# Kernel tuning notes

Hardware: AMD Instinct MI355X
Metric: run time of the kernel (lower is better)

Reference implementation:

```python
import jax, jax.numpy as jnp
import numpy as np
import math

N, S, E, H = 32, 64, 512, 4
HD = E // H
EQ = E // 4
L2_TEMP = 13.544
LN_EPS = 1e-5


def _ln(x, g, b):
    m = jnp.mean(x, -1, keepdims=True)
    v = jnp.var(x, -1, keepdims=True)
    return (x - m) * jax.lax.rsqrt(v + LN_EPS) * g + b


def setup_inputs() -> dict:
    key = jax.random.key(0)
    ks = jax.random.split(key, 16)
    sc = 0.02
    inp = {
        "x": jax.random.normal(ks[0], (N, S, E), jnp.float32),
        # MultiheadAttention params (torch layout: in_proj_weight (3E,E))
        "Wqkv": jax.random.normal(ks[1], (3 * E, E), jnp.float32) * sc,
        "bqkv": jnp.zeros((3 * E,), jnp.float32),
        "Wo": jax.random.normal(ks[2], (E, E), jnp.float32) * sc,
        "bo": jnp.zeros((E,), jnp.float32),
        # fc1 (E, 2E), fc2 (E, E)
        "W1": jax.random.normal(ks[3], (E, 2 * E), jnp.float32) * sc,
        "b1": jnp.zeros((E,), jnp.float32),
        "W2": jax.random.normal(ks[4], (E, E), jnp.float32) * sc,
        "b2": jnp.zeros((E,), jnp.float32),
        # layer norms
        "g1": jnp.ones((E,), jnp.float32), "be1": jnp.zeros((E,), jnp.float32),
        "g2": jnp.ones((E,), jnp.float32), "be2": jnp.zeros((E,), jnp.float32),
        # fc_diff1: Linear(E, E//4), Linear(E//4, 1)
        "d1W1": jax.random.normal(ks[5], (EQ, E), jnp.float32) * sc,
        "d1b1": jnp.zeros((EQ,), jnp.float32),
        "d1W2": jax.random.normal(ks[6], (1, EQ), jnp.float32) * sc,
        "d1b2": jnp.zeros((1,), jnp.float32),
        # fc_diff2
        "d2W1": jax.random.normal(ks[7], (EQ, E), jnp.float32) * sc,
        "d2b1": jnp.zeros((EQ,), jnp.float32),
        "d2W2": jax.random.normal(ks[8], (1, EQ), jnp.float32) * sc,
        "d2b2": jnp.zeros((1,), jnp.float32),
    }
    return inp


def _mha(x, Wqkv, bqkv, Wo, bo):
    n, s, e = x.shape
    qkv = x @ Wqkv.T + bqkv
    q, k, v = jnp.split(qkv, 3, axis=-1)
    sh = lambda t: t.reshape(n, s, H, HD).transpose(0, 2, 1, 3)  # (n,H,s,hd)
    q, k, v = sh(q), sh(k), sh(v)
    scores = jnp.einsum('bhqd,bhkd->bhqk', q, k) / math.sqrt(HD)
    a = jax.nn.softmax(scores, axis=-1)
    o = jnp.einsum('bhqk,bhkd->bhqd', a, v).transpose(0, 2, 1, 3).reshape(n, s, e)
    return o @ Wo.T + bo, a.mean(axis=1)  # averaged attn weights (torch default)


def _pair_mlp(diff_w, W1a, b1a, W2a, b2a):
    # F.relu applied after every 'layer' (Linear, Dropout(eval=id), Linear)
    h = jax.nn.relu(diff_w @ W1a.T + b1a)  # relu(dropout(relu)) == relu composed -> same
    return jax.nn.relu(h @ W2a.T + b2a)[..., 0]  # (N,f,f)


def reference(x, Wqkv, bqkv, Wo, bo, W1, b1, W2, b2, g1, be1, g2, be2,
              d1W1, d1b1, d1W2, d1b2, d2W1, d2b1, d2W2, d2b2):
    # diff[b,f,g,e] = x[b,g,e] - x[b,f,e]
    diff = x[:, None, :, :] - x[:, :, None, :]  # (N,f,f,E)
    x1_attn = jax.nn.softmax(-jnp.sum(diff * diff, -1) / L2_TEMP, axis=-1)  # (N,f,f)
    x1 = jnp.einsum('bfg,bge->bfe', x1_attn, x)
    x2, x2_attn = _mha(x, Wqkv, bqkv, Wo, bo)
    x_res = jnp.concatenate([x1, x2], axis=-1)
    h = x + jax.nn.relu(x_res @ W1.T + b1)  # dropout eval = identity
    h = _ln(h, g1, be1)
    h = h + jax.nn.relu(h @ W2.T + b2)
    out = _ln(h, g2, be2)
    diff1 = _pair_mlp(diff * x1_attn[..., None], d1W1, d1b1, d1W2, d1b2)
    diff2 = _pair_mlp(diff * x2_attn[..., None], d2W1, d2b1, d2W2, d2b2)
    return out, x1_attn[:, None], x2_attn[:, None], diff1, diff2
```

## Files before the change

kernel.cpp:

```cpp
#include <hip/hip_runtime.h>
#include <math.h>

#define SS 64
#define EE 512
#define L2T 13.544f
#define LNEPS 1e-5f

using bf16x8 = __attribute__((ext_vector_type(8))) __bf16;
using u16x8  = __attribute__((ext_vector_type(8))) unsigned short;
using f32x4  = __attribute__((ext_vector_type(4))) float;

typedef const void __attribute__((address_space(1))) cv_global;
typedef void __attribute__((address_space(3))) v_lds;

__device__ inline unsigned short f2bf(float f) {
    union { float f; unsigned u; } v; v.f = f;
    unsigned r = v.u + 0x7fff + ((v.u >> 16) & 1);
    return (unsigned short)(r >> 16);
}
__device__ inline float bf2f(unsigned short h) {
    union { unsigned u; float f; } v; v.u = (unsigned)h << 16;
    return v.f;
}

#define XB_O    0
#define WFULL_O 1048576
#define W1CB_O  1966080
#define W2B_O   2490368
#define QKVB_O  2752512
#define X1O_O   5898240
#define HB_O    7995392
#define PB_O    9043968

__global__ __launch_bounds__(256)
void mega1(const float* __restrict__ x, const float* __restrict__ Wqkv,
           const float* __restrict__ Wo, const float* __restrict__ W1,
           const float* __restrict__ W2, const float* __restrict__ d1,
           const float* __restrict__ d2, const float* __restrict__ b1,
           const float* __restrict__ bo, unsigned short* __restrict__ bb,
           float* __restrict__ b_eff, float* __restrict__ x1_attn) {
    const int bx = blockIdx.x, tid = threadIdx.x;
    __shared__ unsigned short ps[5120];
    __shared__ float l2s[128];

    if (bx < 1408) {
        int i = bx * 256 + tid;
        ushort4* dst4 = (ushort4*)bb;
        const float4* s; int di;
        if (i < 196608)      { s = (const float4*)Wqkv + i;          di = WFULL_O/4 + i; }
        else if (i < 212992) { int j = i-196608; s = (const float4*)d1 + j; di = WFULL_O/4 + 196608 + j; }
        else if (i < 229376) { int j = i-212992; s = (const float4*)d2 + j; di = WFULL_O/4 + 212992 + j; }
        else if (i < 294912) { int j = i-229376; s = (const float4*)W2 + j; di = W2B_O/4 + j; }
        else                 { int j = i-294912; int r = j>>7, cq = j&127;
                               s = (const float4*)W1 + r*256 + cq;   di = W1CB_O/4 + r*256 + cq; }
        float4 v = *s;
        ushort4 o;
        o.x = f2bf(v.x); o.y = f2bf(v.y); o.z = f2bf(v.z); o.w = f2bf(v.w);
        dst4[di] = o;
    } else if (bx < 1472) {
        const int tb = bx - 1408;
        const int m0 = (tb >> 3) * 64, n0 = (tb & 7) * 64;
        unsigned short* Asl = ps;
        unsigned short* Bsl = ps + 64 * 40;
        const int wave = tid >> 6, lane = tid & 63;
        const int wm = (wave >> 1) * 32, wn = (wave & 1) * 32;
        const int fr = lane & 15, kq = (lane >> 4) * 8;
        f32x4 acc[2][2] = {};
        for (int k0 = 0; k0 < 512; k0 += 32) {
            {
                int m = tid >> 2, kk = (tid & 3) * 8;
                const float* src = W1 + (size_t)(m0 + m) * 1024 + 512 + k0 + kk;
                float4 v0 = *(const float4*)src, v1 = *(const float4*)(src + 4);
                u16x8 t = {f2bf(v0.x), f2bf(v0.y), f2bf(v0.z), f2bf(v0.w),
                           f2bf(v1.x), f2bf(v1.y), f2bf(v1.z), f2bf(v1.w)};
                *(u16x8*)(Asl + m * 40 + kk) = t;
            }
            {
                int k = tid >> 3, jq = (tid & 7) * 8;
                const float* src = Wo + (size_t)(k0 + k) * 512 + n0 + jq;
                float4 v0 = *(const float4*)src, v1 = *(const float4*)(src + 4);
                float vv[8] = {v0.x, v0.y, v0.z, v0.w, v1.x, v1.y, v1.z, v1.w};
                #pragma unroll
                for (int e = 0; e < 8; ++e) Bsl[(jq + e) * 40 + k] = f2bf(vv[e]);
            }
            __syncthreads();
            bf16x8 a0 = *(const bf16x8*)(Asl + (wm + fr) * 40 + kq);
            bf16x8 a1 = *(const bf16x8*)(Asl + (wm + 16 + fr) * 40 + kq);
            bf16x8 b0 = *(const bf16x8*)(Bsl + (wn + fr) * 40 + kq);
            bf16x8 b1 = *(const bf16x8*)(Bsl + (wn + 16 + fr) * 40 + kq);
            acc[0][0] = __builtin_amdgcn_mfma_f32_16x16x32_bf16(a0, b0, acc[0][0], 0, 0, 0);
            acc[0][1] = __builtin_amdgcn_mfma_f32_16x16x32_bf16(a0, b1, acc[0][1], 0, 0, 0);
            acc[1][0] = __builtin_amdgcn_mfma_f32_16x16x32_bf16(a1, b0, acc[1][0], 0, 0, 0);
            acc[1][1] = __builtin_amdgcn_mfma_f32_16x16x32_bf16(a1, b1, acc[1][1], 0, 0, 0);
            __syncthreads();
        }
        unsigned short* W1cb = bb + W1CB_O;
        const int crow = (lane >> 4) * 4, ccol = lane & 15;
        #pragma unroll
        for (int r2 = 0; r2 < 2; ++r2)
            #pragma unroll
            for (int c2 = 0; c2 < 2; ++c2)
                #pragma unroll
                for (int i = 0; i < 4; ++i) {
                    int m = m0 + wm + r2 * 16 + crow + i;
                    int j = n0 + wn + c2 * 16 + ccol;
                    W1cb[(size_t)m * 1024 + 512 + j] = f2bf(acc[r2][c2][i]);
                }
    } else if (bx < 1476) {
        int n = (bx - 1472) * 128 + (tid >> 1);
        int kh = (tid & 1) * 256;
        float s = 0.f;
        for (int k = 0; k < 256; ++k)
            s += W1[(size_t)n * 1024 + 512 + kh + k] * bo[kh + k];
        s += __shfl_xor(s, 1);
        if ((tid & 1) == 0) b_eff[n] = b1[n] + s;
    } else {
        const int idx = bx - 1476;
        const int b = idx >> 6, f = idx & 63;
        const int wave = tid >> 6, lane = tid & 63;
        float* d2s = l2s; float* attn_s = l2s + 64;

        const float4* xv = (const float4*)(x + (size_t)b * SS * EE);
        float4 xf0 = xv[f * 128 + lane * 2];
        float4 xf1 = xv[f * 128 + lane * 2 + 1];

        for (int g = wave; g < 64; g += 4) {
            float4 a0 = xv[g * 128 + lane * 2];
            float4 a1 = xv[g * 128 + lane * 2 + 1];
            float dx, s = 0.f;
            dx = a0.x - xf0.x; s += dx * dx;
            dx = a0.y - xf0.y; s += dx * dx;
            dx = a0.z - xf0.z; s += dx * dx;
            dx = a0.w - xf0.w; s += dx * dx;
            dx = a1.x - xf1.x; s += dx * dx;
            dx = a1.y - xf1.y; s += dx * dx;
            dx = a1.z - xf1.z; s += dx * dx;
            dx = a1.w - xf1.w; s += dx * dx;
            #pragma unroll
            for (int m = 32; m; m >>= 1) s += __shfl_xor(s, m);
            if (lane == 0) d2s[g] = s;
        }
        __syncthreads();
        if (tid < 64) {
            float v = -d2s[tid] * (1.0f / L2T);
            float mx = v;
            #pragma unroll
            for (int m = 32; m; m >>= 1) mx = fmaxf(mx, __shfl_xor(mx, m));
            float e = expf(v - mx);
            float sum = e;
            #pragma unroll
            for (int m = 32; m; m >>= 1) sum += __shfl_xor(sum, m);
            float a = e / sum;
            x1_attn[((size_t)b * SS + f) * SS + tid] = a;
            attn_s[tid] = a;
        }
        __syncthreads();
        const float* xbf = x + (size_t)b * SS * EE;
        float acc0 = 0.f, acc1 = 0.f;
        #pragma unroll 8
        for (int g = 0; g < 64; ++g) {
            float ag = attn_s[g];
            acc0 += ag * xbf[g * EE + tid];
            acc1 += ag * xbf[g * EE + tid + 256];
        }
        unsigned short* dst = bb + X1O_O + ((size_t)b * SS + f) * 1024;
        dst[tid] = f2bf(acc0);
        dst[tid + 256] = f2bf(acc1);
        unsigned short* xrow = bb + XB_O + ((size_t)b * SS + f) * EE;
        xrow[tid] = f2bf(xbf[f * EE + tid]);
        xrow[tid + 256] = f2bf(xbf[f * EE + tid + 256]);
    }
}

__global__ __launch_bounds__(256)
void gemm_qkvp(const unsigned short* __restrict__ A,
               const unsigned short* __restrict__ B,
               const float* __restrict__ bias,
               unsigned short* __restrict__ Cq, unsigned short* __restrict__ Cp) {
    __shared__ unsigned short Asl[64 * 64];
    __shared__ unsigned short Bsl[64 * 64];
    const int tid = threadIdx.x, wave = tid >> 6, lane = tid & 63;
    const int m0 = blockIdx.y * 64, n0 = blockIdx.x * 64;
    const int wm = (wave >> 1) * 32, wn = (wave & 1) * 32;
    const int fr = lane & 15, kq4 = lane >> 4;
    f32x4 acc[2][2] = {};

    for (int k0 = 0; k0 < 512; k0 += 64) {
        #pragma unroll
        for (int c0 = 0; c0 < 512; c0 += 256) {
            int cc = c0 + tid, r = cc >> 3, q = cc & 7;
            int col = (q ^ (r & 7)) * 8;
            __builtin_amdgcn_global_load_lds(
                (cv_global*)(A + (size_t)(m0 + r) * 512 + k0 + col),
                (v_lds*)(Asl + c0 * 8 + wave * 512), 16, 0, 0);
        }
        #pragma unroll
        for (int c0 = 0; c0 < 512; c0 += 256) {
            int cc = c0 + tid, r = cc >> 3, q = cc & 7;
            int col = (q ^ (r & 7)) * 8;
            __builtin_amdgcn_global_load_lds(
                (cv_global*)(B + (size_t)(n0 + r) * 512 + k0 + col),
                (v_lds*)(Bsl + c0 * 8 + wave * 512), 16, 0, 0);
        }
        __syncthreads();
        #pragma unroll
        for (int j = 0; j < 2; ++j) {
            int kc = kq4 + j * 4;
            int rb0 = wn + fr, rb1 = wn + 16 + fr;
            bf16x8 b0 = *(const bf16x8*)(Bsl + rb0 * 64 + (kc ^ (rb0 & 7)) * 8);
            bf16x8 b1 = *(const bf16x8*)(Bsl + rb1 * 64 + (kc ^ (rb1 & 7)) * 8);
            #pragma unroll
            for (int r = 0; r < 2; ++r) {
                int ra = wm + r * 16 + fr;
                bf16x8 af = *(const bf16x8*)(Asl + ra * 64 + (kc ^ (ra & 7)) * 8);
                acc[r][0] = __builtin_amdgcn_mfma_f32_16x16x32_bf16(af, b0, acc[r][0], 0, 0, 0);
                acc[r][1] = __builtin_amdgcn_mfma_f32_16x16x32_bf16(af, b1, acc[r][1], 0, 0, 0);
            }
        }
        __syncthreads();
    }

    const int crow = (lane >> 4) * 4, ccol = lane & 15;
    if (blockIdx.x < 24) {
        float bj0 = bias[n0 + wn + ccol], bj1 = bias[n0 + wn + 16 + ccol];
        #pragma unroll
        for (int r = 0; r < 2; ++r)
            #pragma unroll
            for (int c = 0; c < 2; ++c) {
                float bj = c ? bj1 : bj0;
                #pragma unroll
                for (int i = 0; i < 4; ++i) {
                    size_t m = (size_t)(m0 + wm + r * 16 + crow + i);
                    int n = n0 + wn + c * 16 + ccol;
                    Cq[m * 1536 + n] = f2bf(acc[r][c][i] + bj);
                }
            }
    } else {
        int p0 = n0 - 1536;
        #pragma unroll
        for (int r = 0; r < 2; ++r)
            #pragma unroll
            for (int c = 0; c < 2; ++c)
                #pragma unroll
                for (int i = 0; i < 4; ++i) {
                    size_t m = (size_t)(m0 + wm + r * 16 + crow + i);
                    int n = p0 + wn + c * 16 + ccol;
                    Cp[m * 256 + n] = f2bf(acc[r][c][i]);
                }
    }
}

__global__ __launch_bounds__(256)
void mha_attn(const unsigned short* __restrict__ qkv,
              unsigned short* __restrict__ x1o, float* __restrict__ pws) {
    const int hh = blockIdx.x;
    const int h = hh >> 1, half = hh & 1;
    const int b = blockIdx.y;
    const int tid = threadIdx.x, wave = tid >> 6, lane = tid & 63;

    __shared__ unsigned short Qs[32 * 136];
    __shared__ unsigned short Ks[64 * 136];
    __shared__ unsigned short Vt[128 * 72];
    __shared__ float sc[32 * 68];
    __shared__ unsigned short Pbf[32 * 72];

    const unsigned short* base = qkv + (size_t)b * 64 * 1536;
    {
        int row = tid >> 3, col = (tid & 7) * 16;
        const unsigned short* src = base + (half * 32 + row) * 1536 + h * 128 + col;
        *(u16x8*)(Qs + row * 136 + col)     = *(const u16x8*)(src);
        *(u16x8*)(Qs + row * 136 + col + 8) = *(const u16x8*)(src + 8);
    }
    {
        int row = tid >> 2, col = (tid & 3) * 32;
        const unsigned short* src = base + row * 1536 + 512 + h * 128 + col;
        #pragma unroll
        for (int j = 0; j < 4; ++j)
            *(u16x8*)(Ks + row * 136 + col + j * 8) = *(const u16x8*)(src + j * 8);
    }
    {
        int g = tid >> 2, col = (tid & 3) * 32;
        const unsigned short* src = base + g * 1536 + 1024 + h * 128 + col;
        #pragma unroll
        for (int j = 0; j < 4; ++j) {
            u16x8 v = *(const u16x8*)(src + j * 8);
            #pragma unroll
            for (int e = 0; e < 8; ++e)
                Vt[(col + j * 8 + e) * 72 + g] = v[e];
        }
    }
    __syncthreads();

    const int fr = lane & 15, kq = (lane >> 4) * 8;
    const int crow = (lane >> 4) * 4, ccol = lane & 15;
    const int wm = (wave >> 1) * 16;
    {
        const int wn = (wave & 1) * 32;
        f32x4 s0 = {0.f, 0.f, 0.f, 0.f}, s1 = s0;
        #pragma unroll
        for (int k0 = 0; k0 < 128; k0 += 32) {
            bf16x8 a  = *(const bf16x8*)(Qs + (wm + fr) * 136 + k0 + kq);
            bf16x8 b0 = *(const bf16x8*)(Ks + (wn + fr) * 136 + k0 + kq);
            bf16x8 b1 = *(const bf16x8*)(Ks + (wn + 16 + fr) * 136 + k0 + kq);
            s0 = __builtin_amdgcn_mfma_f32_16x16x32_bf16(a, b0, s0, 0, 0, 0);
            s1 = __builtin_amdgcn_mfma_f32_16x16x32_bf16(a, b1, s1, 0, 0, 0);
        }
        const float scale = 0.08838834764831845f;
        #pragma unroll
        for (int r = 0; r < 4; ++r) {
            sc[(wm + crow + r) * 68 + wn + ccol]      = s0[r] * scale;
            sc[(wm + crow + r) * 68 + wn + 16 + ccol] = s1[r] * scale;
        }
    }
    __syncthreads();

    #pragma unroll
    for (int i = 0; i < 8; ++i) {
        int f = wave * 8 + i;
        float v = sc[f * 68 + lane];
        float mx = v;
        #pragma unroll
        for (int m = 32; m; m >>= 1) mx = fmaxf(mx, __shfl_xor(mx, m));
        float e = expf(v - mx);
        float sum = e;
        #pragma unroll
        for (int m = 32; m; m >>= 1) sum += __shfl_xor(sum, m);
        float a = e / sum;
        Pbf[f * 72 + lane] = f2bf(a);
        pws[(((size_t)b * 4 + h) * 64 + half * 32 + f) * 64 + lane] = a;
    }
    __syncthreads();

    {
        const int wn2 = (wave & 1) * 64;
        f32x4 o[4];
        #pragma unroll
        for (int t = 0; t < 4; ++t) o[t] = f32x4{0.f, 0.f, 0.f, 0.f};
        #pragma unroll
        for (int k0 = 0; k0 < 64; k0 += 32) {
            bf16x8 a = *(const bf16x8*)(Pbf + (wm + fr) * 72 + k0 + kq);
            #pragma unroll
            for (int t = 0; t < 4; ++t) {
                bf16x8 bv = *(const bf16x8*)(Vt + (wn2 + t * 16 + fr) * 72 + k0 + kq);
                o[t] = __builtin_amdgcn_mfma_f32_16x16x32_bf16(a, bv, o[t], 0, 0, 0);
            }
        }
        #pragma unroll
        for (int t = 0; t < 4; ++t)
            #pragma unroll
            for (int r = 0; r < 4; ++r) {
                size_t m = (size_t)b * 64 + half * 32 + wm + crow + r;
                int col = h * 128 + wn2 + t * 16 + ccol;
                x1o[m * 1024 + 512 + col] = f2bf(o[t][r]);
            }
    }
}

__global__ __launch_bounds__(256)
void w1pair(const unsigned short* __restrict__ x1o,
            const unsigned short* __restrict__ W1cb,
            const float* __restrict__ beff, float* __restrict__ u,
            const unsigned short* __restrict__ Pb,
            const float* __restrict__ a1, const float* __restrict__ pws,
            const float* __restrict__ d1b1, const float* __restrict__ d1w2,
            const float* __restrict__ d1b2, const float* __restrict__ d2b1,
            const float* __restrict__ d2w2, const float* __restrict__ d2b2,
            float* __restrict__ x2_attn, float* __restrict__ out1,
            float* __restrict__ out2) {
    __shared__ unsigned short Asl[32 * 64];
    __shared__ unsigned short Bsl[64 * 64];
    const int bx = blockIdx.x, tid = threadIdx.x;
    const int wave = tid >> 6, lane = tid & 63;

    if (bx < 512) {
        const int m0 = (bx >> 3) * 32, n0 = (bx & 7) * 64;
        const int wm = (wave >> 1) * 16, wn = (wave & 1) * 32;
        const int fr = lane & 15, kq4 = lane >> 4;
        f32x4 acc[2] = {};
        for (int k0 = 0; k0 < 1024; k0 += 64) {
            {
                int r = tid >> 3, q = tid & 7;
                int col = (q ^ (r & 7)) * 8;
                __builtin_amdgcn_global_load_lds(
                    (cv_global*)(x1o + (size_t)(m0 + r) * 1024 + k0 + col),
                    (v_lds*)(Asl + wave * 512), 16, 0, 0);
            }
            #pragma unroll
            for (int c0 = 0; c0 < 512; c0 += 256) {
                int cc = c0 + tid, r = cc >> 3, q = cc & 7;
                int col = (q ^ (r & 7)) * 8;
                __builtin_amdgcn_global_load_lds(
                    (cv_global*)(W1cb + (size_t)(n0 + r) * 1024 + k0 + col),
                    (v_lds*)(Bsl + c0 * 8 + wave * 512), 16, 0, 0);
            }
            __syncthreads();
            #pragma unroll
            for (int j = 0; j < 2; ++j) {
                int kc = kq4 + j * 4;
                int rb0 = wn + fr, rb1 = wn + 16 + fr, ra = wm + fr;
                bf16x8 b0 = *(const bf16x8*)(Bsl + rb0 * 64 + (kc ^ (rb0 & 7)) * 8);
                bf16x8 b1 = *(const bf16x8*)(Bsl + rb1 * 64 + (kc ^ (rb1 & 7)) * 8);
                bf16x8 af = *(const bf16x8*)(Asl + ra * 64 + (kc ^ (ra & 7)) * 8);
                acc[0] = __builtin_amdgcn_mfma_f32_16x16x32_bf16(af, b0, acc[0], 0, 0, 0);
                acc[1] = __builtin_amdgcn_mfma_f32_16x16x32_bf16(af, b1, acc[1], 0, 0, 0);
            }
            __syncthreads();
        }
        const int crow = (lane >> 4) * 4, ccol = lane & 15;
        #pragma unroll
        for (int c = 0; c < 2; ++c) {
            int n = n0 + wn + c * 16 + ccol;
            float bj = beff[n];
            #pragma unroll
            for (int i = 0; i < 4; ++i) {
                size_t m = (size_t)(m0 + wm + crow + i);
                u[m * 512 + n] = fmaxf(acc[c][i] + bj, 0.f);
            }
        }
    } else {
        const int idx = bx - 512;
        const int f = idx & 63, b = idx >> 6;
        const size_t row = (size_t)b * SS + f;
        const int c0 = lane * 2, c1 = lane * 2 + 1;

        const float p1f0 = bf2f(Pb[row * 256 + c0]),       p1f1 = bf2f(Pb[row * 256 + c1]);
        const float p2f0 = bf2f(Pb[row * 256 + 128 + c0]), p2f1 = bf2f(Pb[row * 256 + 128 + c1]);
        const float w10 = d1w2[c0], w11 = d1w2[c1];
        const float w20 = d2w2[c0], w21 = d2w2[c1];
        const float b10 = d1b1[c0], b11 = d1b1[c1];
        const float b20 = d2b1[c0], b21 = d2b1[c1];
        const float bb1 = d1b2[0], bb2 = d2b2[0];

        const float* a1r = a1 + row * SS;
        const float* ph0 = pws + (((size_t)b * 4 + 0) * 64 + f) * 64;
        const float* ph1 = pws + (((size_t)b * 4 + 1) * 64 + f) * 64;
        const float* ph2 = pws + (((size_t)b * 4 + 2) * 64 + f) * 64;
        const float* ph3 = pws + (((size_t)b * 4 + 3) * 64 + f) * 64;
        const size_t bbase = (size_t)b * SS * 256;

        for (int g = wave; g < 64; g += 4) {
            float aa1 = a1r[g];
            float aa2 = 0.25f * (ph0[g] + ph1[g] + ph2[g] + ph3[g]);
            float q10 = bf2f(Pb[bbase + g * 256 + c0]);
            float q11 = bf2f(Pb[bbase + g * 256 + c1]);
            float q20 = bf2f(Pb[bbase + g * 256 + 128 + c0]);
            float q21 = bf2f(Pb[bbase + g * 256 + 128 + c1]);
            float h10 = fmaxf(aa1 * (q10 - p1f0) + b10, 0.f);
            float h11 = fmaxf(aa1 * (q11 - p1f1) + b11, 0.f);
            float h20 = fmaxf(aa2 * (q20 - p2f0) + b20, 0.f);
            float h21 = fmaxf(aa2 * (q21 - p2f1) + b21, 0.f);
            float s1 = w10 * h10 + w11 * h11;
            float s2 = w20 * h20 + w21 * h21;
            #pragma unroll
            for (int m = 32; m; m >>= 1) {
                s1 += __shfl_xor(s1, m);
                s2 += __shfl_xor(s2, m);
            }
            if (lane == 0) {
                x2_attn[row * SS + g] = aa2;
                out1[row * SS + g] = fmaxf(s1 + bb1, 0.f);
                out2[row * SS + g] = fmaxf(s2 + bb2, 0.f);
            }
        }
    }
}

__global__ __launch_bounds__(256)
void gemm_w2(const unsigned short* __restrict__ A,
             const unsigned short* __restrict__ B,
             const float* __restrict__ bias, float* __restrict__ C) {
    __shared__ unsigned short Asl[32 * 64];
    __shared__ unsigned short Bsl[64 * 64];
    const int tid = threadIdx.x, wave = tid >> 6, lane = tid & 63;
    const int m0 = blockIdx.y * 32, n0 = blockIdx.x * 64;
    const int wm = (wave >> 1) * 16, wn = (wave & 1) * 32;
    const int fr = lane & 15, kq4 = lane >> 4;
    f32x4 acc[2] = {};
    for (int k0 = 0; k0 < 512; k0 += 64) {
        {
            int r = tid >> 3, q = tid & 7;
            int col = (q ^ (r & 7)) * 8;
            __builtin_amdgcn_global_load_lds(
                (cv_global*)(A + (size_t)(m0 + r) * 512 + k0 + col),
                (v_lds*)(Asl + wave * 512), 16, 0, 0);
        }
        #pragma unroll
        for (int c0 = 0; c0 < 512; c0 += 256) {
            int cc = c0 + tid, r = cc >> 3, q = cc & 7;
            int col = (q ^ (r & 7)) * 8;
            __builtin_amdgcn_global_load_lds(
                (cv_global*)(B + (size_t)(n0 + r) * 512 + k0 + col),
                (v_lds*)(Bsl + c0 * 8 + wave * 512), 16, 0, 0);
        }
        __syncthreads();
        #pragma unroll
        for (int j = 0; j < 2; ++j) {
            int kc = kq4 + j * 4;
            int rb0 = wn + fr, rb1 = wn + 16 + fr, ra = wm + fr;
            bf16x8 b0 = *(const bf16x8*)(Bsl + rb0 * 64 + (kc ^ (rb0 & 7)) * 8);
            bf16x8 b1 = *(const bf16x8*)(Bsl + rb1 * 64 + (kc ^ (rb1 & 7)) * 8);
            bf16x8 af = *(const bf16x8*)(Asl + ra * 64 + (kc ^ (ra & 7)) * 8);
            acc[0] = __builtin_amdgcn_mfma_f32_16x16x32_bf16(af, b0, acc[0], 0, 0, 0);
            acc[1] = __builtin_amdgcn_mfma_f32_16x16x32_bf16(af, b1, acc[1], 0, 0, 0);
        }
        __syncthreads();
    }
    const int crow = (lane >> 4) * 4, ccol = lane & 15;
    #pragma unroll
    for (int c = 0; c < 2; ++c) {
        int n = n0 + wn + c * 16 + ccol;
        float bj = bias[n];
        #pragma unroll
        for (int i = 0; i < 4; ++i) {
            size_t m = (size_t)(m0 + wm + crow + i);
            C[m * 512 + n] = fmaxf(acc[c][i] + bj, 0.f);
        }
    }
}

__global__ __launch_bounds__(256)
void add_ln(const float* __restrict__ base, const float* __restrict__ u,
            const float* __restrict__ gam, const float* __restrict__ bet,
            float* __restrict__ out, unsigned short* __restrict__ outb) {
    const int row = blockIdx.x;
    const int tid = threadIdx.x, wave = tid >> 6, lane = tid & 63;
    const float* br = base + (size_t)row * EE;
    const float* ur = u + (size_t)row * EE;
    float t0 = br[tid] + ur[tid];
    float t1 = br[tid + 256] + ur[tid + 256];
    float s = t0 + t1, sq = t0 * t0 + t1 * t1;
    #pragma unroll
    for (int m = 32; m; m >>= 1) {
        s += __shfl_xor(s, m);
        sq += __shfl_xor(sq, m);
    }
    __shared__ float ssum[4], ssq[4];
    if (lane == 0) { ssum[wave] = s; ssq[wave] = sq; }
    __syncthreads();
    s = ssum[0] + ssum[1] + ssum[2] + ssum[3];
    sq = ssq[0] + ssq[1] + ssq[2] + ssq[3];
    float mean = s * (1.0f / EE);
    float var = sq * (1.0f / EE) - mean * mean;
    float inv = rsqrtf(var + LNEPS);
    float v0 = (t0 - mean) * inv * gam[tid] + bet[tid];
    float v1 = (t1 - mean) * inv * gam[tid + 256] + bet[tid + 256];
    float* orow = out + (size_t)row * EE;
    orow[tid] = v0;
    orow[tid + 256] = v1;
    if (outb) {
        unsigned short* obr = outb + (size_t)row * EE;
        obr[tid] = f2bf(v0);
        obr[tid + 256] = f2bf(v1);
    }
}

extern "C" void kernel_launch(void* const* d_in, const int* in_sizes, int n_in,
                              void* d_out, int out_size, void* d_ws,
                              size_t ws_size, hipStream_t stream) {
    const float* x    = (const float*)d_in[0];
    const float* Wqkv = (const float*)d_in[1];
    const float* bqkv = (const float*)d_in[2];
    const float* Wo   = (const float*)d_in[3];
    const float* bo   = (const float*)d_in[4];
    const float* W1   = (const float*)d_in[5];
    const float* b1   = (const float*)d_in[6];
    const float* W2   = (const float*)d_in[7];
    const float* b2   = (const float*)d_in[8];
    const float* g1   = (const float*)d_in[9];
    const float* be1  = (const float*)d_in[10];
    const float* g2   = (const float*)d_in[11];
    const float* be2  = (const float*)d_in[12];
    const float* d1W1 = (const float*)d_in[13];
    const float* d1b1 = (const float*)d_in[14];
    const float* d1W2 = (const float*)d_in[15];
    const float* d1b2 = (const float*)d_in[16];
    const float* d2W1 = (const float*)d_in[17];
    const float* d2b1 = (const float*)d_in[18];
    const float* d2W2 = (const float*)d_in[19];
    const float* d2b2 = (const float*)d_in[20];

    float* out      = (float*)d_out;
    float* out_main = out;
    float* x1_attn  = out + 1048576;
    float* x2_attn  = out + 1048576 + 131072;
    float* diff1    = out + 1048576 + 2 * 131072;
    float* diff2    = out + 1048576 + 3 * 131072;

    float* ws    = (float*)d_ws;
    float* u_buf = ws;
    float* h_buf = ws + 1048576;
    float* pws   = ws + 2097152;
    float* b_eff = ws + 2621440;
    unsigned short* bb = (unsigned short*)(ws + 2621952);

    unsigned short* xb    = bb + XB_O;
    unsigned short* Wfull = bb + WFULL_O;
    unsigned short* W1cb  = bb + W1CB_O;
    unsigned short* W2b   = bb + W2B_O;
    unsigned short* qkvb  = bb + QKVB_O;
    unsigned short* x1o   = bb + X1O_O;
    unsigned short* hb    = bb + HB_O;
    unsigned short* Pb    = bb + PB_O;

    mega1<<<3524, 256, 0, stream>>>(x, Wqkv, Wo, W1, W2, d1W1, d2W1, b1, bo,
                                    bb, b_eff, x1_attn);

    gemm_qkvp<<<dim3(28, 32), 256, 0, stream>>>(xb, Wfull, bqkv, qkvb, Pb);

    mha_attn<<<dim3(8, 32), 256, 0, stream>>>(qkvb, x1o, pws);

    w1pair<<<2560, 256, 0, stream>>>(x1o, W1cb, b_eff, u_buf, Pb, x1_attn, pws,
                                     d1b1, d1W2, d1b2, d2b1, d2W2, d2b2,
                                     x2_attn, diff1, diff2);

    add_ln<<<2048, 256, 0, stream>>>(x, u_buf, g1, be1, h_buf, hb);

    gemm_w2<<<dim3(8, 64), 256, 0, stream>>>(hb, W2b, b2, u_buf);

    add_ln<<<2048, 256, 0, stream>>>(h_buf, u_buf, g2, be2, out_main, nullptr);
}
```

Before: 191.2 us.

## Compute L2 attention via split-bf16 Gram MFMA and move x1 matmul into QKV kernel

The pairwise squared-distance path now runs one block per batch. It builds the 64x64 Gram matrix of x with MFMA, splitting each value into hi and lo bf16 parts (three products) to keep precision, and forms distances as norm_f + norm_g - 2*dot. This replaces 2048 per-row blocks that each reread the batch's rows from global memory. The softmax weights are stored as bf16, and the attention-weighted sum x1 = attn @ x is computed by extra MFMA blocks in the QKV GEMM launch. The cost is some precision loss from the norm expansion and bf16 weights, and a larger shared-memory footprint per block.

```diff
diff --git a/kernel.cpp b/kernel.cpp
--- a/kernel.cpp
+++ b/kernel.cpp
@@ -22,6 +22,8 @@
     union { unsigned u; float f; } v; v.u = (unsigned)h << 16;
     return v.f;
 }
+
+#define MFMA16 __builtin_amdgcn_mfma_f32_16x16x32_bf16
 
 #define XB_O    0
 #define WFULL_O 1048576
@@ -38,10 +40,10 @@
            const float* __restrict__ W2, const float* __restrict__ d1,
            const float* __restrict__ d2, const float* __restrict__ b1,
            const float* __restrict__ bo, unsigned short* __restrict__ bb,
-           float* __restrict__ b_eff, float* __restrict__ x1_attn) {
+           float* __restrict__ b_eff, float* __restrict__ x1_attn,
+           unsigned short* __restrict__ Pl2) {
     const int bx = blockIdx.x, tid = threadIdx.x;
-    __shared__ unsigned short ps[5120];
-    __shared__ float l2s[128];
+    __shared__ __align__(16) char smem[36096];
 
     if (bx < 1408) {
         int i = bx * 256 + tid;
@@ -60,8 +62,8 @@
     } else if (bx < 1472) {
         const int tb = bx - 1408;
         const int m0 = (tb >> 3) * 64, n0 = (tb & 7) * 64;
-        unsigned short* Asl = ps;
-        unsigned short* Bsl = ps + 64 * 40;
+        unsigned short* Asl = (unsigned short*)smem;
+        unsigned short* Bsl = Asl + 64 * 40;
         const int wave = tid >> 6, lane = tid & 63;
         const int wm = (wave >> 1) * 32, wn = (wave & 1) * 32;
         const int fr = lane & 15, kq = (lane >> 4) * 8;
@@ -88,10 +90,10 @@
             bf16x8 a1 = *(const bf16x8*)(Asl + (wm + 16 + fr) * 40 + kq);
             bf16x8 b0 = *(const bf16x8*)(Bsl + (wn + fr) * 40 + kq);
             bf16x8 b1 = *(const bf16x8*)(Bsl + (wn + 16 + fr) * 40 + kq);
-            acc[0][0] = __builtin_amdgcn_mfma_f32_16x16x32_bf16(a0, b0, acc[0][0], 0, 0, 0);
-            acc[0][1] = __builtin_amdgcn_mfma_f32_16x16x32_bf16(a0, b1, acc[0][1], 0, 0, 0);
-            acc[1][0] = __builtin_amdgcn_mfma_f32_16x16x32_bf16(a1, b0, acc[1][0], 0, 0, 0);
-            acc[1][1] = __builtin_amdgcn_mfma_f32_16x16x32_bf16(a1, b1, acc[1][1], 0, 0, 0);
+            acc[0][0] = MFMA16(a0, b0, acc[0][0], 0, 0, 0);
+            acc[0][1] = MFMA16(a0, b1, acc[0][1], 0, 0, 0);
+            acc[1][0] = MFMA16(a1, b0, acc[1][0], 0, 0, 0);
+            acc[1][1] = MFMA16(a1, b1, acc[1][1], 0, 0, 0);
             __syncthreads();
         }
         unsigned short* W1cb = bb + W1CB_O;
@@ -115,60 +117,96 @@
         s += __shfl_xor(s, 1);
         if ((tid & 1) == 0) b_eff[n] = b1[n] + s;
     } else {
-        const int idx = bx - 1476;
-        const int b = idx >> 6, f = idx & 63;
+        const int b = bx - 1476;
+        unsigned short* Xhi = (unsigned short*)smem;
+        unsigned short* Xlo = Xhi + 64 * 72;
+        float* sc    = (float*)(Xlo + 64 * 72);
+        float* norms = sc + 64 * 68;
         const int wave = tid >> 6, lane = tid & 63;
-        float* d2s = l2s; float* attn_s = l2s + 64;
-
-        const float4* xv = (const float4*)(x + (size_t)b * SS * EE);
-        float4 xf0 = xv[f * 128 + lane * 2];
-        float4 xf1 = xv[f * 128 + lane * 2 + 1];
-
-        for (int g = wave; g < 64; g += 4) {
-            float4 a0 = xv[g * 128 + lane * 2];
-            float4 a1 = xv[g * 128 + lane * 2 + 1];
-            float dx, s = 0.f;
-            dx = a0.x - xf0.x; s += dx * dx;
-            dx = a0.y - xf0.y; s += dx * dx;
-            dx = a0.z - xf0.z; s += dx * dx;
-            dx = a0.w - xf0.w; s += dx * dx;
-            dx = a1.x - xf1.x; s += dx * dx;
-            dx = a1.y - xf1.y; s += dx * dx;
-            dx = a1.z - xf1.z; s += dx * dx;
-            dx = a1.w - xf1.w; s += dx * dx;
-            #pragma unroll
-            for (int m = 32; m; m >>= 1) s += __shfl_xor(s, m);
-            if (lane == 0) d2s[g] = s;
-        }
+        const int wm = (wave >> 1) * 32, wn = (wave & 1) * 32;
+        const int fr = lane & 15;
+        const int srow = tid >> 2, scq = (tid & 3) * 16;
+
+        f32x4 acc[2][2] = {};
+        const float* xrow = x + (size_t)b * 32768;
+        unsigned short* xbg = bb + XB_O + (size_t)b * 32768;
+
+        for (int k0 = 0; k0 < 512; k0 += 64) {
+            const float* src = xrow + srow * 512 + k0 + scq;
+            u16x8 hi0, hi1, lo0, lo1;
+            #pragma unroll
+            for (int e = 0; e < 8; ++e) {
+                float v = src[e];
+                unsigned short h = f2bf(v);
+                hi0[e] = h; lo0[e] = f2bf(v - bf2f(h));
+            }
+            #pragma unroll
+            for (int e = 0; e < 8; ++e) {
+                float v = src[8 + e];
+                unsigned short h = f2bf(v);
+                hi1[e] = h; lo1[e] = f2bf(v - bf2f(h));
+            }
+            *(u16x8*)(Xhi + srow * 72 + scq)     = hi0;
+            *(u16x8*)(Xhi + srow * 72 + scq + 8) = hi1;
+            *(u16x8*)(Xlo + srow * 72 + scq)     = lo0;
+            *(u16x8*)(Xlo + srow * 72 + scq + 8) = lo1;
+            *(u16x8*)(xbg + srow * 512 + k0 + scq)     = hi0;
+            *(u16x8*)(xbg + srow * 512 + k0 + scq + 8) = hi1;
+            __syncthreads();
+            #pragma unroll
+            for (int j = 0; j < 2; ++j) {
+                int kk = j * 32 + (lane >> 4) * 8;
+                bf16x8 ah0 = *(const bf16x8*)(Xhi + (wm + fr) * 72 + kk);
+                bf16x8 ah1 = *(const bf16x8*)(Xhi + (wm + 16 + fr) * 72 + kk);
+                bf16x8 bh0 = *(const bf16x8*)(Xhi + (wn + fr) * 72 + kk);
+                bf16x8 bh1 = *(const bf16x8*)(Xhi + (wn + 16 + fr) * 72 + kk);
+                bf16x8 al0 = *(const bf16x8*)(Xlo + (wm + fr) * 72 + kk);
+                bf16x8 al1 = *(const bf16x8*)(Xlo + (wm + 16 + fr) * 72 + kk);
+                bf16x8 bl0 = *(const bf16x8*)(Xlo + (wn + fr) * 72 + kk);
+                bf16x8 bl1 = *(const bf16x8*)(Xlo + (wn + 16 + fr) * 72 + kk);
+                acc[0][0] = MFMA16(ah0, bh0, acc[0][0], 0, 0, 0);
+                acc[0][0] = MFMA16(ah0, bl0, acc[0][0], 0, 0, 0);
+                acc[0][0] = MFMA16(al0, bh0, acc[0][0], 0, 0, 0);
+                acc[0][1] = MFMA16(ah0, bh1, acc[0][1], 0, 0, 0);
+                acc[0][1] = MFMA16(ah0, bl1, acc[0][1], 0, 0, 0);
+                acc[0][1] = MFMA16(al0, bh1, acc[0][1], 0, 0, 0);
+                acc[1][0] = MFMA16(ah1, bh0, acc[1][0], 0, 0, 0);
+                acc[1][0] = MFMA16(ah1, bl0, acc[1][0], 0, 0, 0);
+                acc[1][0] = MFMA16(al1, bh0, acc[1][0], 0, 0, 0);
+                acc[1][1] = MFMA16(ah1, bh1, acc[1][1], 0, 0, 0);
+                acc[1][1] = MFMA16(ah1, bl1, acc[1][1], 0, 0, 0);
+                acc[1][1] = MFMA16(al1, bh1, acc[1][1], 0, 0, 0);
+            }
+            __syncthreads();
+        }
+        const int crow = (lane >> 4) * 4, ccol = lane & 15;
+        #pragma unroll
+        for (int r2 = 0; r2 < 2; ++r2)
+            #pragma unroll
+            for (int c2 = 0; c2 < 2; ++c2)
+                #pragma unroll
+                for (int i = 0; i < 4; ++i)
+                    sc[(wm + r2 * 16 + crow + i) * 68 + wn + c2 * 16 + ccol] =
+                        acc[r2][c2][i];
         __syncthreads();
-        if (tid < 64) {
-            float v = -d2s[tid] * (1.0f / L2T);
-            float mx = v;
+        if (tid < 64) norms[tid] = sc[tid * 68 + tid];
+        __syncthreads();
+        #pragma unroll
+        for (int i = 0; i < 16; ++i) {
+            int f = wave * 16 + i;
+            float nf = norms[f];
+            float val = (2.f * sc[f * 68 + lane] - nf - norms[lane]) * (1.0f / L2T);
+            float mx = val;
             #pragma unroll
             for (int m = 32; m; m >>= 1) mx = fmaxf(mx, __shfl_xor(mx, m));
-            float e = expf(v - mx);
+            float e = expf(val - mx);
             float sum = e;
             #pragma unroll
             for (int m = 32; m; m >>= 1) sum += __shfl_xor(sum, m);
             float a = e / sum;
-            x1_attn[((size_t)b * SS + f) * SS + tid] = a;
-            attn_s[tid] = a;
-        }
-        __syncthreads();
-        const float* xbf = x + (size_t)b * SS * EE;
-        float acc0 = 0.f, acc1 = 0.f;
-        #pragma unroll 8
-        for (int g = 0; g < 64; ++g) {
-            float ag = attn_s[g];
-            acc0 += ag * xbf[g * EE + tid];
-            acc1 += ag * xbf[g * EE + tid + 256];
-        }
-        unsigned short* dst = bb + X1O_O + ((size_t)b * SS + f) * 1024;
-        dst[tid] = f2bf(acc0);
-        dst[tid + 256] = f2bf(acc1);
-        unsigned short* xrow = bb + XB_O + ((size_t)b * SS + f) * EE;
-        xrow[tid] = f2bf(xbf[f * EE + tid]);
-        xrow[tid + 256] = f2bf(xbf[f * EE + tid + 256]);
+            x1_attn[((size_t)b * 64 + f) * 64 + lane] = a;
+            Pl2[((size_t)b * 64 + f) * 64 + lane] = f2bf(a);
+        }
     }
 }
 
@@ -176,77 +214,124 @@
 void gemm_qkvp(const unsigned short* __restrict__ A,
                const unsigned short* __restrict__ B,
                const float* __restrict__ bias,
-               unsigned short* __restrict__ Cq, unsigned short* __restrict__ Cp) {
-    __shared__ unsigned short Asl[64 * 64];
-    __shared__ unsigned short Bsl[64 * 64];
+               unsigned short* __restrict__ Cq, unsigned short* __restrict__ Cp,
+               const unsigned short* __restrict__ Pl2,
+               unsigned short* __restrict__ x1o) {
+    __shared__ unsigned short qsm[8704];
     const int tid = threadIdx.x, wave = tid >> 6, lane = tid & 63;
-    const int m0 = blockIdx.y * 64, n0 = blockIdx.x * 64;
-    const int wm = (wave >> 1) * 32, wn = (wave & 1) * 32;
-    const int fr = lane & 15, kq4 = lane >> 4;
-    f32x4 acc[2][2] = {};
-
-    for (int k0 = 0; k0 < 512; k0 += 64) {
-        #pragma unroll
-        for (int c0 = 0; c0 < 512; c0 += 256) {
-            int cc = c0 + tid, r = cc >> 3, q = cc & 7;
-            int col = (q ^ (r & 7)) * 8;
-            __builtin_amdgcn_global_load_lds(
-                (cv_global*)(A + (size_t)(m0 + r) * 512 + k0 + col),
-                (v_lds*)(Asl + c0 * 8 + wave * 512), 16, 0, 0);
-        }
-        #pragma unroll
-        for (int c0 = 0; c0 < 512; c0 += 256) {
-            int cc = c0 + tid, r = cc >> 3, q = cc & 7;
-            int col = (q ^ (r & 7)) * 8;
-            __builtin_amdgcn_global_load_lds(
-                (cv_global*)(B + (size_t)(n0 + r) * 512 + k0 + col),
-                (v_lds*)(Bsl + c0 * 8 + wave * 512), 16, 0, 0);
+    const int fr = lane & 15;
+    const int crow = (lane >> 4) * 4, ccol = lane & 15;
+
+    if (blockIdx.x < 28) {
+        unsigned short* Asl = qsm;
+        unsigned short* Bsl = qsm + 4096;
+        const int m0 = blockIdx.y * 64, n0 = blockIdx.x * 64;
+        const int wm = (wave >> 1) * 32, wn = (wave & 1) * 32;
+        const int kq4 = lane >> 4;
+        f32x4 acc[2][2] = {};
+
+        for (int k0 = 0; k0 < 512; k0 += 64) {
+            #pragma unroll
+            for (int c0 = 0; c0 < 512; c0 += 256) {
+                int cc = c0 + tid, r = cc >> 3, q = cc & 7;
+                int col = (q ^ (r & 7)) * 8;
+                __builtin_amdgcn_global_load_lds(
+                    (cv_global*)(A + (size_t)(m0 + r) * 512 + k0 + col),
+                    (v_lds*)(Asl + c0 * 8 + wave * 512), 16, 0, 0);
+            }
+            #pragma unroll
+            for (int c0 = 0; c0 < 512; c0 += 256) {
+                int cc = c0 + tid, r = cc >> 3, q = cc & 7;
+                int col = (q ^ (r & 7)) * 8;
+                __builtin_amdgcn_global_load_lds(
+                    (cv_global*)(B + (size_t)(n0 + r) * 512 + k0 + col),
+                    (v_lds*)(Bsl + c0 * 8 + wave * 512), 16, 0, 0);
+            }
+            __syncthreads();
+            #pragma unroll
+            for (int j = 0; j < 2; ++j) {
+                int kc = kq4 + j * 4;
+                int rb0 = wn + fr, rb1 = wn + 16 + fr;
+                bf16x8 b0 = *(const bf16x8*)(Bsl + rb0 * 64 + (kc ^ (rb0 & 7)) * 8);
+                bf16x8 b1 = *(const bf16x8*)(Bsl + rb1 * 64 + (kc ^ (rb1 & 7)) * 8);
+                #pragma unroll
+                for (int r = 0; r < 2; ++r) {
+                    int ra = wm + r * 16 + fr;
+                    bf16x8 af = *(const bf16x8*)(Asl + ra * 64 + (kc ^ (ra & 7)) * 8);
+                    acc[r][0] = MFMA16(af, b0, acc[r][0], 0, 0, 0);
+                    acc[r][1] = MFMA16(af, b1, acc[r][1], 0, 0, 0);
+                }
+            }
+            __syncthreads();
+        }
+
+        if (blockIdx.x < 24) {
+            float bj0 = bias[n0 + wn + ccol], bj1 = bias[n0 + wn + 16 + ccol];
+            #pragma unroll
+            for (int r = 0; r < 2; ++r)
+                #pragma unroll
+                for (int c = 0; c < 2; ++c) {
+                    float bj = c ? bj1 : bj0;
+                    #pragma unroll
+                    for (int i = 0; i < 4; ++i) {
+                        size_t m = (size_t)(m0 + wm + r * 16 + crow + i);
+                        int n = n0 + wn + c * 16 + ccol;
+                        Cq[m * 1536 + n] = f2bf(acc[r][c][i] + bj);
+                    }
+                }
+        } else {
+            int p0 = n0 - 1536;
+            #pragma unroll
+            for (int r = 0; r < 2; ++r)
+                #pragma unroll
+                for (int c = 0; c < 2; ++c)
+                    #pragma unroll
+                    for (int i = 0; i < 4; ++i) {
+                        size_t m = (size_t)(m0 + wm + r * 16 + crow + i);
+                        int n = p0 + wn + c * 16 + ccol;
+                        Cp[m * 256 + n] = f2bf(acc[r][c][i]);
+                    }
+        }
+    } else {
+        const int e0 = (blockIdx.x - 28) * 64;
+        const int b = blockIdx.y;
+        unsigned short* Ap = qsm;
+        unsigned short* Xt = qsm + 64 * 68;
+        {
+            int row = tid >> 2, cq = (tid & 3) * 16;
+            const unsigned short* src = Pl2 + (size_t)b * 4096 + row * 64 + cq;
+            *(u16x8*)(Ap + row * 68 + cq)     = *(const u16x8*)src;
+            *(u16x8*)(Ap + row * 68 + cq + 8) = *(const u16x8*)(src + 8);
+        }
+        {
+            int g = tid >> 2, cq = (tid & 3) * 16;
+            const unsigned short* src = A + (size_t)b * 32768 + g * 512 + e0 + cq;
+            u16x8 v0 = *(const u16x8*)src, v1 = *(const u16x8*)(src + 8);
+            #pragma unroll
+            for (int e = 0; e < 8; ++e) Xt[(cq + e) * 68 + g] = v0[e];
+            #pragma unroll
+            for (int e = 0; e < 8; ++e) Xt[(cq + 8 + e) * 68 + g] = v1[e];
         }
         __syncthreads();
+        const int wm2 = wave * 16;
+        f32x4 o[4] = {};
         #pragma unroll
         for (int j = 0; j < 2; ++j) {
-            int kc = kq4 + j * 4;
-            int rb0 = wn + fr, rb1 = wn + 16 + fr;
-            bf16x8 b0 = *(const bf16x8*)(Bsl + rb0 * 64 + (kc ^ (rb0 & 7)) * 8);
-            bf16x8 b1 = *(const bf16x8*)(Bsl + rb1 * 64 + (kc ^ (rb1 & 7)) * 8);
-            #pragma unroll
-            for (int r = 0; r < 2; ++r) {
-                int ra = wm + r * 16 + fr;
-                bf16x8 af = *(const bf16x8*)(Asl + ra * 64 + (kc ^ (ra & 7)) * 8);
-                acc[r][0] = __builtin_amdgcn_mfma_f32_16x16x32_bf16(af, b0, acc[r][0], 0, 0, 0);
-                acc[r][1] = __builtin_amdgcn_mfma_f32_16x16x32_bf16(af, b1, acc[r][1], 0, 0, 0);
-            }
-        }
-        __syncthreads();
-    }
-
-    const int crow = (lane >> 4) * 4, ccol = lane & 15;
-    if (blockIdx.x < 24) {
-        float bj0 = bias[n0 + wn + ccol], bj1 = bias[n0 + wn + 16 + ccol];
-        #pragma unroll
-        for (int r = 0; r < 2; ++r)
-            #pragma unroll
-            for (int c = 0; c < 2; ++c) {
-                float bj = c ? bj1 : bj0;
-                #pragma unroll
-                for (int i = 0; i < 4; ++i) {
-                    size_t m = (size_t)(m0 + wm + r * 16 + crow + i);
-                    int n = n0 + wn + c * 16 + ccol;
-                    Cq[m * 1536 + n] = f2bf(acc[r][c][i] + bj);
-                }
-            }
-    } else {
-        int p0 = n0 - 1536;
-        #pragma unroll
-        for (int r = 0; r < 2; ++r)
-            #pragma unroll
-            for (int c = 0; c < 2; ++c)
-                #pragma unroll
-                for (int i = 0; i < 4; ++i) {
-                    size_t m = (size_t)(m0 + wm + r * 16 + crow + i);
-                    int n = p0 + wn + c * 16 + ccol;
-                    Cp[m * 256 + n] = f2bf(acc[r][c][i]);
-                }
+            int kk = j * 32 + (lane >> 4) * 8;
+            bf16x8 a = *(const bf16x8*)(Ap + (wm2 + fr) * 68 + kk);
+            #pragma unroll
+            for (int t = 0; t < 4; ++t) {
+                bf16x8 bv = *(const bf16x8*)(Xt + (t * 16 + fr) * 68 + kk);
+                o[t] = MFMA16(a, bv, o[t], 0, 0, 0);
+            }
+        }
+        #pragma unroll
+        for (int t = 0; t < 4; ++t)
+            #pragma unroll
+            for (int i = 0; i < 4; ++i) {
+                size_t m = (size_t)b * 64 + wm2 + crow + i;
+                x1o[m * 1024 + e0 + t * 16 + ccol] = f2bf(o[t][i]);
+            }
     }
 }
 
@@ -302,8 +387,8 @@
             bf16x8 a  = *(const bf16x8*)(Qs + (wm + fr) * 136 + k0 + kq);
             bf16x8 b0 = *(const bf16x8*)(Ks + (wn + fr) * 136 + k0 + kq);
             bf16x8 b1 = *(const bf16x8*)(Ks + (wn + 16 + fr) * 136 + k0 + kq);
-            s0 = __builtin_amdgcn_mfma_f32_16x16x32_bf16(a, b0, s0, 0, 0, 0);
-            s1 = __builtin_amdgcn_mfma_f32_16x16x32_bf16(a, b1, s1, 0, 0, 0);
+            s0 = MFMA16(a, b0, s0, 0, 0, 0);
+            s1 = MFMA16(a, b1, s1, 0, 0, 0);
         }
         const float scale = 0.08838834764831845f;
         #pragma unroll
@@ -342,7 +427,7 @@
             #pragma unroll
             for (int t = 0; t < 4; ++t) {
                 bf16x8 bv = *(const bf16x8*)(Vt + (wn2 + t * 16 + fr) * 72 + k0 + kq);
-                o[t] = __builtin_amdgcn_mfma_f32_16x16x32_bf16(a, bv, o[t], 0, 0, 0);
+                o[t] = MFMA16(a, bv, o[t], 0, 0, 0);
             }
         }
         #pragma unroll
@@ -401,8 +486,8 @@
                 bf16x8 b0 = *(const bf16x8*)(Bsl + rb0 * 64 + (kc ^ (rb0 & 7)) * 8);
                 bf16x8 b1 = *(const bf16x8*)(Bsl + rb1 * 64 + (kc ^ (rb1 & 7)) * 8);
                 bf16x8 af = *(const bf16x8*)(Asl + ra * 64 + (kc ^ (ra & 7)) * 8);
-                acc[0] = __builtin_amdgcn_mfma_f32_16x16x32_bf16(af, b0, acc[0], 0, 0, 0);
-                acc[1] = __builtin_amdgcn_mfma_f32_16x16x32_bf16(af, b1, acc[1], 0, 0, 0);
+                acc[0] = MFMA16(af, b0, acc[0], 0, 0, 0);
+                acc[1] = MFMA16(af, b1, acc[1], 0, 0, 0);
             }
             __syncthreads();
         }
@@ -500,8 +585,8 @@
             bf16x8 b0 = *(const bf16x8*)(Bsl + rb0 * 64 + (kc ^ (rb0 & 7)) * 8);
             bf16x8 b1 = *(const bf16x8*)(Bsl + rb1 * 64 + (kc ^ (rb1 & 7)) * 8);
             bf16x8 af = *(const bf16x8*)(Asl + ra * 64 + (kc ^ (ra & 7)) * 8);
-            acc[0] = __builtin_amdgcn_mfma_f32_16x16x32_bf16(af, b0, acc[0], 0, 0, 0);
-            acc[1] = __builtin_amdgcn_mfma_f32_16x16x32_bf16(af, b1, acc[1], 0, 0, 0);
+            acc[0] = MFMA16(af, b0, acc[0], 0, 0, 0);
+            acc[1] = MFMA16(af, b1, acc[1], 0, 0, 0);
         }
         __syncthreads();
     }
@@ -591,7 +676,8 @@
     float* h_buf = ws + 1048576;
     float* pws   = ws + 2097152;
     float* b_eff = ws + 2621440;
-    unsigned short* bb = (unsigned short*)(ws + 2621952);
+    unsigned short* Pl2 = (unsigned short*)(ws + 2621952);
+    unsigned short* bb  = (unsigned short*)(ws + 2687488);
 
     unsigned short* xb    = bb + XB_O;
     unsigned short* Wfull = bb + WFULL_O;
@@ -602,10 +688,11 @@
     unsigned short* hb    = bb + HB_O;
     unsigned short* Pb    = bb + PB_O;
 
-    mega1<<<3524, 256, 0, stream>>>(x, Wqkv, Wo, W1, W2, d1W1, d2W1, b1, bo,
-                                    bb, b_eff, x1_attn);
-
-    gemm_qkvp<<<dim3(28, 32), 256, 0, stream>>>(xb, Wfull, bqkv, qkvb, Pb);
+    mega1<<<1508, 256, 0, stream>>>(x, Wqkv, Wo, W1, W2, d1W1, d2W1, b1, bo,
+                                    bb, b_eff, x1_attn, Pl2);
+
+    gemm_qkvp<<<dim3(36, 32), 256, 0, stream>>>(xb, Wfull, bqkv, qkvb, Pb,
+                                                Pl2, x1o);
 
     mha_attn<<<dim3(8, 32), 256, 0, stream>>>(qkvb, x1o, pws);
 
```

Result: faster. 179.0 us (-6.4%).
